# Optimization experiments

Hardware: AMD Instinct MI355X
Metric: run time of the kernel (lower is better)

## Reference

```python
import jax, jax.numpy as jnp
import numpy as np

H = W = 64      # input_resolution
WS = 8          # window_size
NH = 8          # num_heads
C = 256         # dim
HD = C // NH    # head_dim
SCALE = HD ** -0.5
N = WS * WS     # tokens per window
EPS = 1e-5


def _layernorm(x, g, b):
    m = jnp.mean(x, axis=-1, keepdims=True)
    v = jnp.var(x, axis=-1, keepdims=True)
    return (x - m) * jax.lax.rsqrt(v + EPS) * g + b


def _rel_pos_index():
    # Swin relative position index for a WSxWS window -> (N, N) int array
    coords = np.stack(np.meshgrid(np.arange(WS), np.arange(WS), indexing='ij'))  # (2,WS,WS)
    cf = coords.reshape(2, -1)                      # (2, N)
    rel = cf[:, :, None] - cf[:, None, :]           # (2, N, N)
    rel = rel.transpose(1, 2, 0).astype(np.int64)   # (N, N, 2)
    rel[:, :, 0] += WS - 1
    rel[:, :, 1] += WS - 1
    rel[:, :, 0] *= 2 * WS - 1
    return jnp.asarray(rel.sum(-1))                 # (N, N)


def _window_partition(x, B):
    # x: (B, H, W, C) -> (B*nW, N, C)
    x = x.reshape(B, H // WS, WS, W // WS, WS, C)
    x = x.transpose(0, 1, 3, 2, 4, 5)
    return x.reshape(-1, N, C)


def setup_inputs() -> dict:
    key = jax.random.key(0)
    ks = jax.random.split(key, 8)
    B = 16
    std = 0.02
    return {
        'x1': jax.random.normal(ks[0], (B, H * W, C), jnp.float32),
        'x2': jax.random.normal(ks[1], (B, H * W, C), jnp.float32),
        'norm1_g': jnp.ones((C,), jnp.float32),
        'norm1_b': jnp.zeros((C,), jnp.float32),
        'q_w': jax.random.normal(ks[2], (C, C), jnp.float32) * std,
        'q_b': jnp.zeros((C,), jnp.float32),
        'kv_w': jax.random.normal(ks[3], (C, 2 * C), jnp.float32) * std,
        'kv_b': jnp.zeros((2 * C,), jnp.float32),
        'proj_w': jax.random.normal(ks[4], (C, C), jnp.float32) * std,
        'proj_b': jnp.zeros((C,), jnp.float32),
        'rel_table': jax.random.normal(ks[5], ((2 * WS - 1) ** 2, NH), jnp.float32) * std,
        'norm3_g': jnp.ones((C,), jnp.float32),
        'norm3_b': jnp.zeros((C,), jnp.float32),
        'fc1_w': jax.random.normal(ks[6], (C, 4 * C), jnp.float32) * std,
        'fc1_b': jnp.zeros((4 * C,), jnp.float32),
        'fc2_w': jax.random.normal(ks[7], (4 * C, C), jnp.float32) * std,
        'fc2_b': jnp.zeros((C,), jnp.float32),
    }


def reference(x1, x2, norm1_g, norm1_b, q_w, q_b, kv_w, kv_b, proj_w, proj_b,
              rel_table, norm3_g, norm3_b, fc1_w, fc1_b, fc2_w, fc2_b):
    B = x1.shape[0]
    shortcut = x1
    # norm1 applied to both streams (as in source)
    x1n = _layernorm(x1, norm1_g, norm1_b).reshape(B, H, W, C)
    x2n = _layernorm(x2, norm1_g, norm1_b).reshape(B, H, W, C)
    x1w = _window_partition(x1n, B)  # (B_, N, C)
    x2w = _window_partition(x2n, B)  # (B_, N, C)
    B_ = x1w.shape[0]

    q = (x1w @ q_w + q_b).reshape(B_, N, NH, HD).transpose(0, 2, 1, 3)      # (B_,h,N,d)
    kv = (x2w @ kv_w + kv_b).reshape(B_, N, 2, NH, HD)
    k = kv[:, :, 0].transpose(0, 2, 1, 3)                                    # (B_,h,N,d)
    v = kv[:, :, 1].transpose(0, 2, 1, 3)                                    # (B_,h,N,d)

    attn = jnp.einsum('bhnd,bhmd->bhnm', q * SCALE, k)                       # (B_,h,N,N)
    bias = rel_table[_rel_pos_index().reshape(-1)].reshape(N, N, NH)
    attn = jax.nn.softmax(attn + bias.transpose(2, 0, 1)[None], axis=-1)

    out = jnp.einsum('bhnm,bhmd->bhnd', attn, v)
    out = out.transpose(0, 2, 1, 3).reshape(B_, N, C) @ proj_w + proj_b      # (B_,N,C)

    # window reverse -> (B, H*W, C)
    xr = out.reshape(B, H // WS, W // WS, WS, WS, C)
    xr = xr.transpose(0, 1, 3, 2, 4, 5).reshape(B, H * W, C)

    x = shortcut + xr
    h = _layernorm(x, norm3_g, norm3_b)
    h = jax.nn.gelu(h @ fc1_w + fc1_b, approximate=False) @ fc2_w + fc2_b
    return x + h
```

## Files before the change

kernel.cpp:

```cpp
#include <hip/hip_runtime.h>

typedef __bf16 bf16x8 __attribute__((ext_vector_type(8)));
typedef float f32x4 __attribute__((ext_vector_type(4)));
using u16 = unsigned short;

#define SCALE 0.17677669529663689f
#define XROW 528

__device__ __forceinline__ u16 f2bf(float f) {
    union { __bf16 h; u16 u; } x; x.h = (__bf16)f; return x.u;
}
__device__ __forceinline__ unsigned pk2(float a, float b) {
    union { struct { __bf16 lo, hi; } s; unsigned u; } x;
    x.s.lo = (__bf16)a; x.s.hi = (__bf16)b; return x.u;
}
__device__ __forceinline__ float bf2f(u16 h) {
    union { unsigned u; float f; } x; x.u = ((unsigned)h) << 16; return x.f;
}
__device__ __forceinline__ float gelu_s(float x) {
    float u = 2.3022150048054216f * x * (1.f + 0.044715f * x * x);
    float e = exp2f(-u);
    return x / (1.f + e);
}

__global__ __launch_bounds__(256) void prep_k(
    const float* __restrict__ q_w, const float* __restrict__ kv_w,
    const float* __restrict__ p_w, const float* __restrict__ f1w,
    const float* __restrict__ f2w, const float* __restrict__ rel,
    u16* __restrict__ qp, u16* __restrict__ kvp, u16* __restrict__ pp,
    u16* __restrict__ f1p, u16* __restrict__ f2p, float* __restrict__ biasF)
{
    int t = blockIdx.x * 256 + threadIdx.x;
    if (t < 65536) {
        int u = t;
        int e = u & 7, l = (u >> 3) & 63, ks = (u >> 9) & 7, ng = u >> 12;
        int k = ks * 32 + (l >> 4) * 8 + e;
        int n = ng * 16 + (l & 15);
        qp[u] = f2bf(q_w[k * 256 + n]);
    } else if (t < 196608) {
        int u = t - 65536;
        int e = u & 7, l = (u >> 3) & 63, ks = (u >> 9) & 7, ng = u >> 12;
        int k = ks * 32 + (l >> 4) * 8 + e;
        int n = ng * 16 + (l & 15);
        kvp[u] = f2bf(kv_w[k * 512 + n]);
    } else if (t < 262144) {
        int u = t - 196608;
        int e = u & 7, l = (u >> 3) & 63, ks = (u >> 9) & 7, ng = u >> 12;
        int k = ks * 32 + (l >> 4) * 8 + e;
        int n = ng * 16 + (l & 15);
        pp[u] = f2bf(p_w[k * 256 + n]);
    } else if (t < 524288) {
        int u = t - 262144;
        int e = u & 7, l = (u >> 3) & 63, ks = (u >> 9) & 7, ng = u >> 12;
        int k = ks * 32 + (l >> 4) * 8 + e;
        int n = ng * 16 + (l & 15);
        f1p[u] = f2bf(f1w[k * 1024 + n]);
    } else if (t < 786432) {
        int u = t - 524288;
        int e = u & 7, l = (u >> 3) & 63, ks = (u >> 9) & 31, ng = u >> 14;
        int k = ks * 32 + (l >> 4) * 8 + e;
        int n = ng * 16 + (l & 15);
        f2p[u] = f2bf(f2w[k * 256 + n]);
    } else if (t < 819200) {
        int u = t - 786432;
        int r = u & 3, l = (u >> 2) & 63, fr = (u >> 8) & 15, h = u >> 12;
        int fi = fr >> 2, fj = fr & 3;
        int m = fi * 16 + (l & 15);
        int n = fj * 16 + 4 * (l >> 4) + r;
        int idx = ((m >> 3) - (n >> 3) + 7) * 15 + ((m & 7) - (n & 7) + 7);
        biasF[u] = rel[idx * 8 + h];
    }
}

#define LN_ROW16(SRCP, GG, BB, OUT0, OUT1)                                    \
    {                                                                         \
        float4 v0 = *(const float4*)(SRCP);                                   \
        float4 v1 = *(const float4*)(SRCP + 4);                               \
        float4 v2 = *(const float4*)(SRCP + 8);                               \
        float4 v3 = *(const float4*)(SRCP + 12);                              \
        float s = (v0.x + v0.y + v0.z + v0.w) + (v1.x + v1.y + v1.z + v1.w)   \
                + (v2.x + v2.y + v2.z + v2.w) + (v3.x + v3.y + v3.z + v3.w);  \
        float q = v0.x*v0.x + v0.y*v0.y + v0.z*v0.z + v0.w*v0.w               \
                + v1.x*v1.x + v1.y*v1.y + v1.z*v1.z + v1.w*v1.w               \
                + v2.x*v2.x + v2.y*v2.y + v2.z*v2.z + v2.w*v2.w               \
                + v3.x*v3.x + v3.y*v3.y + v3.z*v3.z + v3.w*v3.w;              \
        _Pragma("unroll")                                                     \
        for (int m_ = 1; m_ <= 8; m_ <<= 1) {                                 \
            s += __shfl_xor(s, m_, 64);                                       \
            q += __shfl_xor(q, m_, 64);                                       \
        }                                                                     \
        float mean = s * (1.0f / 256.0f);                                     \
        float rstd = rsqrtf(q * (1.0f / 256.0f) - mean * mean + 1e-5f);       \
        uint4 o0_, o1_;                                                       \
        o0_.x = pk2((v0.x-mean)*rstd*GG[0].x+BB[0].x, (v0.y-mean)*rstd*GG[0].y+BB[0].y); \
        o0_.y = pk2((v0.z-mean)*rstd*GG[0].z+BB[0].z, (v0.w-mean)*rstd*GG[0].w+BB[0].w); \
        o0_.z = pk2((v1.x-mean)*rstd*GG[1].x+BB[1].x, (v1.y-mean)*rstd*GG[1].y+BB[1].y); \
        o0_.w = pk2((v1.z-mean)*rstd*GG[1].z+BB[1].z, (v1.w-mean)*rstd*GG[1].w+BB[1].w); \
        o1_.x = pk2((v2.x-mean)*rstd*GG[2].x+BB[2].x, (v2.y-mean)*rstd*GG[2].y+BB[2].y); \
        o1_.y = pk2((v2.z-mean)*rstd*GG[2].z+BB[2].z, (v2.w-mean)*rstd*GG[2].w+BB[2].w); \
        o1_.z = pk2((v3.x-mean)*rstd*GG[3].x+BB[3].x, (v3.y-mean)*rstd*GG[3].y+BB[3].y); \
        o1_.w = pk2((v3.z-mean)*rstd*GG[3].z+BB[3].z, (v3.w-mean)*rstd*GG[3].w+BB[3].w); \
        OUT0 = o0_; OUT1 = o1_;                                               \
    }

__global__ __launch_bounds__(512, 3) void attn_mega(
    const float* __restrict__ x1, const float* __restrict__ x2,
    const float* __restrict__ gw, const float* __restrict__ bw,
    const bf16x8* __restrict__ qp, const bf16x8* __restrict__ kvp,
    const float* __restrict__ q_b, const float* __restrict__ kv_b,
    const float* __restrict__ biasF, const bf16x8* __restrict__ pp,
    const float* __restrict__ p_b, u16* __restrict__ xbw)
{
    __shared__ __align__(16) char SMEM[74752];
    u16* Xl0  = (u16*)SMEM;
    u16* Xl1  = (u16*)(SMEM + 33792);
    u16* VtA  = (u16*)SMEM;
    u16* Olds = (u16*)(SMEM + 40960);
    const int t = threadIdx.x, lane = t & 63, w = t >> 6;
    const int g = lane >> 4, c = lane & 15;
    const int win = blockIdx.x;
    const int b_ = win >> 6, wh = (win >> 3) & 7, ww = win & 7;

    {
        const int ln_sub = lane >> 4, ln_c = lane & 15;
        float4 GG[4], BB[4];
        #pragma unroll
        for (int j = 0; j < 4; j++) {
            GG[j] = *(const float4*)(gw + ln_c * 16 + j * 4);
            BB[j] = *(const float4*)(bw + ln_c * 16 + j * 4);
        }
        #pragma unroll
        for (int it = 0; it < 4; it++) {
            int idx = w * 16 + it * 4 + ln_sub;
            int st = idx >> 6, n = idx & 63;
            const float* src = st ? x2 : x1;
            size_t srow = (size_t)b_ * 4096 + (wh * 8 + (n >> 3)) * 64 + ww * 8 + (n & 7);
            const float* p = src + srow * 256 + ln_c * 16;
            uint4 o0, o1;
            LN_ROW16(p, GG, BB, o0, o1)
            u16* dst = st ? Xl1 : Xl0;
            char* base = (char*)dst + n * XROW + ln_c * 32;
            *(uint4*)(base) = o0;
            *(uint4*)(base + 16) = o1;
        }
    }
    __syncthreads();

    const int srcA = c + 16 * ((2 * g) & 3);
    const int srcB = srcA + 16;
    const bool nhi = (g >= 2);

#define GEMM256(acc, WPTR, NGBASE, XSRC)                                      \
    { _Pragma("unroll")                                                       \
      for (int i = 0; i < 4; i++) { acc[i][0] = (f32x4){0,0,0,0};             \
                                    acc[i][1] = (f32x4){0,0,0,0}; }           \
      _Pragma("unroll")                                                       \
      for (int ks = 0; ks < 8; ks++) {                                        \
          bf16x8 wf[2], af[4];                                                \
          _Pragma("unroll")                                                   \
          for (int n = 0; n < 2; n++)                                         \
              wf[n] = WPTR[(size_t)(((NGBASE) + n) * 8 + ks) * 64 + lane];    \
          _Pragma("unroll")                                                   \
          for (int i = 0; i < 4; i++)                                         \
              af[i] = *(const bf16x8*)((char*)XSRC + (i * 16 + c) * XROW      \
                                       + g * 16 + ks * 64);                   \
          __builtin_amdgcn_s_setprio(1);                                      \
          _Pragma("unroll")                                                   \
          for (int i = 0; i < 4; i++)                                         \
              _Pragma("unroll")                                               \
              for (int n = 0; n < 2; n++)                                     \
                  acc[i][n] = __builtin_amdgcn_mfma_f32_16x16x32_bf16(        \
                      wf[n], af[i], acc[i][n], 0, 0, 0);                      \
          __builtin_amdgcn_s_setprio(0);                                      \
      } }

#define ADDBIAS(acc, BPTR, CBASE)                                             \
    { _Pragma("unroll")                                                       \
      for (int i = 0; i < 4; i++)                                             \
          _Pragma("unroll")                                                   \
          for (int n = 0; n < 2; n++) {                                       \
              float4 b4 = *(const float4*)((BPTR) + (CBASE) + n * 16 + 4 * g);\
              acc[i][n][0] += b4.x; acc[i][n][1] += b4.y;                     \
              acc[i][n][2] += b4.z; acc[i][n][3] += b4.w;                     \
          } }

#define REPACK(acc, frag)                                                     \
    { unsigned w0_[4][2], w1_[4][2];                                          \
      _Pragma("unroll")                                                       \
      for (int i = 0; i < 4; i++)                                             \
          _Pragma("unroll")                                                   \
          for (int n = 0; n < 2; n++) {                                       \
              w0_[i][n] = pk2(acc[i][n][0], acc[i][n][1]);                    \
              w1_[i][n] = pk2(acc[i][n][2], acc[i][n][3]);                    \
          }                                                                   \
      _Pragma("unroll")                                                       \
      for (int i = 0; i < 4; i++) {                                           \
          unsigned x0a = __shfl(w0_[i][0], srcA), x0b = __shfl(w0_[i][1], srcA);\
          unsigned y0a = __shfl(w1_[i][0], srcA), y0b = __shfl(w1_[i][1], srcA);\
          unsigned x1a = __shfl(w0_[i][0], srcB), x1b = __shfl(w0_[i][1], srcB);\
          unsigned y1a = __shfl(w1_[i][0], srcB), y1b = __shfl(w1_[i][1], srcB);\
          union { uint4 u; bf16x8 v; } cv;                                    \
          cv.u.x = nhi ? x0b : x0a;                                           \
          cv.u.y = nhi ? y0b : y0a;                                           \
          cv.u.z = nhi ? x1b : x1a;                                           \
          cv.u.w = nhi ? y1b : y1a;                                           \
          frag[i] = cv.v;                                                     \
      } }

    bf16x8 qf[4], kf[4];
    f32x4 av[4][2];
    {
        f32x4 acc[4][2];
        GEMM256(acc, kvp, 2 * w, Xl1)
        ADDBIAS(acc, kv_b, w * 32)
        REPACK(acc, kf)
        GEMM256(acc, qp, 2 * w, Xl0)
        ADDBIAS(acc, q_b, w * 32)
        REPACK(acc, qf)
        GEMM256(av, kvp, 16 + 2 * w, Xl1)
        ADDBIAS(av, kv_b, 256 + w * 32)
    }
    __syncthreads();

    u16* vt = VtA + w * 32 * 80;
    #pragma unroll
    for (int i = 0; i < 4; i++)
        #pragma unroll
        for (int n = 0; n < 2; n++)
            #pragma unroll
            for (int r = 0; r < 4; r++)
                vt[(n * 16 + 4 * g + r) * 80 + i * 16 + c] = f2bf(av[i][n][r]);

    f32x4 s[4][4];
    #pragma unroll
    for (int i = 0; i < 4; i++)
        #pragma unroll
        for (int j = 0; j < 4; j++) {
            s[i][j] = (f32x4){0.f, 0.f, 0.f, 0.f};
            s[i][j] = __builtin_amdgcn_mfma_f32_16x16x32_bf16(kf[j], qf[i], s[i][j], 0, 0, 0);
        }

    #pragma unroll
    for (int i = 0; i < 4; i++)
        #pragma unroll
        for (int j = 0; j < 4; j++) {
            f32x4 bf4 = *(const f32x4*)(biasF + ((size_t)(w * 16 + i * 4 + j) * 64 + lane) * 4);
            #pragma unroll
            for (int r = 0; r < 4; r++) s[i][j][r] = s[i][j][r] * SCALE + bf4[r];
        }

    #pragma unroll
    for (int i = 0; i < 4; i++) {
        float mx = -1e30f;
        #pragma unroll
        for (int j = 0; j < 4; j++)
            #pragma unroll
            for (int r = 0; r < 4; r++) mx = fmaxf(mx, s[i][j][r]);
        mx = fmaxf(mx, __shfl_xor(mx, 16, 64));
        mx = fmaxf(mx, __shfl_xor(mx, 32, 64));
        float sum = 0.f;
        #pragma unroll
        for (int j = 0; j < 4; j++)
            #pragma unroll
            for (int r = 0; r < 4; r++) {
                float e = __expf(s[i][j][r] - mx);
                s[i][j][r] = e; sum += e;
            }
        sum += __shfl_xor(sum, 16, 64);
        sum += __shfl_xor(sum, 32, 64);
        float inv = 1.f / sum;
        #pragma unroll
        for (int j = 0; j < 4; j++)
            #pragma unroll
            for (int r = 0; r < 4; r++) s[i][j][r] *= inv;
    }

    unsigned pw0[4][4], pw1[4][4];
    #pragma unroll
    for (int i = 0; i < 4; i++)
        #pragma unroll
        for (int j = 0; j < 4; j++) {
            pw0[i][j] = pk2(s[i][j][0], s[i][j][1]);
            pw1[i][j] = pk2(s[i][j][2], s[i][j][3]);
        }
    f32x4 o[4][2];
    #pragma unroll
    for (int i = 0; i < 4; i++) { o[i][0] = (f32x4){0,0,0,0}; o[i][1] = (f32x4){0,0,0,0}; }
    #pragma unroll
    for (int ks = 0; ks < 2; ks++) {
        bf16x8 pa[4], vb[2];
        #pragma unroll
        for (int i = 0; i < 4; i++) {
            unsigned a0 = __shfl(pw0[i][2 * ks], srcA), b0 = __shfl(pw0[i][2 * ks + 1], srcA);
            unsigned a1 = __shfl(pw1[i][2 * ks], srcA), b1 = __shfl(pw1[i][2 * ks + 1], srcA);
            unsigned a2 = __shfl(pw0[i][2 * ks], srcB), b2 = __shfl(pw0[i][2 * ks + 1], srcB);
            unsigned a3 = __shfl(pw1[i][2 * ks], srcB), b3 = __shfl(pw1[i][2 * ks + 1], srcB);
            union { uint4 u; bf16x8 v; } cv;
            cv.u.x = nhi ? b0 : a0;
            cv.u.y = nhi ? b1 : a1;
            cv.u.z = nhi ? b2 : a2;
            cv.u.w = nhi ? b3 : a3;
            pa[i] = cv.v;
        }
        #pragma unroll
        for (int j = 0; j < 2; j++) {
            int d = j * 16 + c;
            vb[j] = *(const bf16x8*)(vt + d * 80 + ks * 32 + 8 * g);
        }
        #pragma unroll
        for (int i = 0; i < 4; i++)
            #pragma unroll
            for (int j = 0; j < 2; j++)
                o[i][j] = __builtin_amdgcn_mfma_f32_16x16x32_bf16(vb[j], pa[i], o[i][j], 0, 0, 0);
    }

    #pragma unroll
    for (int i = 0; i < 4; i++) {
        int row = i * 16 + c;
        #pragma unroll
        for (int j = 0; j < 2; j++) {
            uint2 pk = { pk2(o[i][j][0], o[i][j][1]), pk2(o[i][j][2], o[i][j][3]) };
            *(uint2*)((char*)Olds + row * XROW + w * 64 + j * 32 + g * 8) = pk;
        }
    }
    __syncthreads();

    f32x4 ap[4][2];
    #pragma unroll
    for (int i = 0; i < 4; i++) { ap[i][0] = (f32x4){0,0,0,0}; ap[i][1] = (f32x4){0,0,0,0}; }
    #pragma unroll
    for (int ks = 0; ks < 8; ks++) {
        bf16x8 wf[2], ah[4];
        #pragma unroll
        for (int n = 0; n < 2; n++)
            wf[n] = pp[(size_t)((w * 2 + n) * 8 + ks) * 64 + lane];
        #pragma unroll
        for (int i = 0; i < 4; i++)
            ah[i] = *(const bf16x8*)((char*)Olds + (i * 16 + c) * XROW
                                     + g * 16 + ks * 64);
        __builtin_amdgcn_s_setprio(1);
        #pragma unroll
        for (int i = 0; i < 4; i++)
            #pragma unroll
            for (int n = 0; n < 2; n++)
                ap[i][n] = __builtin_amdgcn_mfma_f32_16x16x32_bf16(
                    wf[n], ah[i], ap[i][n], 0, 0, 0);
        __builtin_amdgcn_s_setprio(0);
    }

    #pragma unroll
    for (int i = 0; i < 4; i++) {
        int n = i * 16 + c;
        size_t nrow = (size_t)b_ * 4096 + (wh * 8 + (n >> 3)) * 64 + ww * 8 + (n & 7);
        #pragma unroll
        for (int j = 0; j < 2; j++) {
            int col = w * 32 + j * 16 + 4 * g;
            float4 b4 = *(const float4*)(p_b + col);
            float4 r4 = *(const float4*)(x1 + nrow * 256 + col);
            uint2 pk = { pk2(ap[i][j][0] + b4.x + r4.x, ap[i][j][1] + b4.y + r4.y),
                         pk2(ap[i][j][2] + b4.z + r4.z, ap[i][j][3] + b4.w + r4.w) };
            *(uint2*)(xbw + nrow * 256 + col) = pk;
        }
    }
#undef GEMM256
#undef ADDBIAS
#undef REPACK
}

__global__ __launch_bounds__(512, 4) void mlp_mega(
    const u16* __restrict__ xb, const float* __restrict__ gw,
    const float* __restrict__ bw, const bf16x8* __restrict__ f1p,
    const bf16x8* __restrict__ f2p, const float* __restrict__ f1b,
    const float* __restrict__ f2b, float* __restrict__ out)
{
    __shared__ __align__(16) u16 Xl[64 * 264];
    __shared__ __align__(16) u16 Hl[64 * 264];
    const int t = threadIdx.x, lane = t & 63, w = t >> 6;
    const int g = lane >> 4, c = lane & 15;
    const int m0 = blockIdx.x * 64;

    {
        const int ln_sub = lane >> 4, ln_c = lane & 15;
        float4 GG[4], BB[4];
        #pragma unroll
        for (int j = 0; j < 4; j++) {
            GG[j] = *(const float4*)(gw + ln_c * 16 + j * 4);
            BB[j] = *(const float4*)(bw + ln_c * 16 + j * 4);
        }
        #pragma unroll
        for (int it = 0; it < 2; it++) {
            int row = w * 8 + it * 4 + ln_sub;
            const u16* p = xb + (size_t)(m0 + row) * 256 + ln_c * 16;
            uint4 rv = *(const uint4*)(p);
            uint4 rw = *(const uint4*)(p + 8);
            float v[16];
            v[0] = bf2f((u16)rv.x);  v[1] = bf2f((u16)(rv.x >> 16));
            v[2] = bf2f((u16)rv.y);  v[3] = bf2f((u16)(rv.y >> 16));
            v[4] = bf2f((u16)rv.z);  v[5] = bf2f((u16)(rv.z >> 16));
            v[6] = bf2f((u16)rv.w);  v[7] = bf2f((u16)(rv.w >> 16));
            v[8] = bf2f((u16)rw.x);  v[9] = bf2f((u16)(rw.x >> 16));
            v[10] = bf2f((u16)rw.y); v[11] = bf2f((u16)(rw.y >> 16));
            v[12] = bf2f((u16)rw.z); v[13] = bf2f((u16)(rw.z >> 16));
            v[14] = bf2f((u16)rw.w); v[15] = bf2f((u16)(rw.w >> 16));
            float s = 0.f, q = 0.f;
            #pragma unroll
            for (int e = 0; e < 16; e++) { s += v[e]; q += v[e] * v[e]; }
            #pragma unroll
            for (int m_ = 1; m_ <= 8; m_ <<= 1) {
                s += __shfl_xor(s, m_, 64);
                q += __shfl_xor(q, m_, 64);
            }
            float mean = s * (1.0f / 256.0f);
            float rstd = rsqrtf(q * (1.0f / 256.0f) - mean * mean + 1e-5f);
            uint4 o0, o1;
            const float* G = (const float*)GG;
            const float* B = (const float*)BB;
            o0.x = pk2((v[0]-mean)*rstd*G[0]+B[0],  (v[1]-mean)*rstd*G[1]+B[1]);
            o0.y = pk2((v[2]-mean)*rstd*G[2]+B[2],  (v[3]-mean)*rstd*G[3]+B[3]);
            o0.z = pk2((v[4]-mean)*rstd*G[4]+B[4],  (v[5]-mean)*rstd*G[5]+B[5]);
            o0.w = pk2((v[6]-mean)*rstd*G[6]+B[6],  (v[7]-mean)*rstd*G[7]+B[7]);
            o1.x = pk2((v[8]-mean)*rstd*G[8]+B[8],  (v[9]-mean)*rstd*G[9]+B[9]);
            o1.y = pk2((v[10]-mean)*rstd*G[10]+B[10],(v[11]-mean)*rstd*G[11]+B[11]);
            o1.z = pk2((v[12]-mean)*rstd*G[12]+B[12],(v[13]-mean)*rstd*G[13]+B[13]);
            o1.w = pk2((v[14]-mean)*rstd*G[14]+B[14],(v[15]-mean)*rstd*G[15]+B[15]);
            char* base = (char*)Xl + row * XROW + ln_c * 32;
            *(uint4*)(base) = o0;
            *(uint4*)(base + 16) = o1;
        }
    }
    __syncthreads();

    f32x4 acc2[4][2];
    #pragma unroll
    for (int i = 0; i < 4; i++) { acc2[i][0] = (f32x4){0,0,0,0}; acc2[i][1] = (f32x4){0,0,0,0}; }

    #pragma unroll
    for (int hc = 0; hc < 4; hc++) {
        f32x4 acc1[4][2];
        #pragma unroll
        for (int i = 0; i < 4; i++) { acc1[i][0] = (f32x4){0,0,0,0}; acc1[i][1] = (f32x4){0,0,0,0}; }

        const bf16x8* f1base = f1p + (size_t)((hc * 16 + w * 2) * 8) * 64 + lane;
        bf16x8 wA[2], wB[2];
        #pragma unroll
        for (int n = 0; n < 2; n++) wA[n] = f1base[(n * 8 + 0) * 64];

#define FC1_STEP(WREG, ks_)                                                   \
        {                                                                     \
            bf16x8 af[4];                                                     \
            _Pragma("unroll")                                                 \
            for (int i = 0; i < 4; i++)                                       \
                af[i] = *(const bf16x8*)((char*)Xl + (i * 16 + c) * XROW      \
                                         + g * 16 + (ks_) * 64);             \
            __builtin_amdgcn_s_setprio(1);                                    \
            _Pragma("unroll")                                                 \
            for (int i = 0; i < 4; i++)                                       \
                _Pragma("unroll")                                             \
                for (int n = 0; n < 2; n++)                                   \
                    acc1[i][n] = __builtin_amdgcn_mfma_f32_16x16x32_bf16(     \
                        WREG[n], af[i], acc1[i][n], 0, 0, 0);                 \
            __builtin_amdgcn_s_setprio(0);                                    \
        }

        #pragma unroll
        for (int ks = 0; ks < 8; ks += 2) {
            #pragma unroll
            for (int n = 0; n < 2; n++) wB[n] = f1base[(n * 8 + ks + 1) * 64];
            FC1_STEP(wA, ks)
            if (ks + 2 < 8) {
                #pragma unroll
                for (int n = 0; n < 2; n++) wA[n] = f1base[(n * 8 + ks + 2) * 64];
            }
            FC1_STEP(wB, ks + 1)
        }
#undef FC1_STEP

        #pragma unroll
        for (int i = 0; i < 4; i++) {
            int row = i * 16 + c;
            #pragma unroll
            for (int n = 0; n < 2; n++) {
                float4 b4 = *(const float4*)(f1b + hc * 256 + w * 32 + n * 16 + 4 * g);
                float h0 = gelu_s(acc1[i][n][0] + b4.x);
                float h1 = gelu_s(acc1[i][n][1] + b4.y);
                float h2 = gelu_s(acc1[i][n][2] + b4.z);
                float h3 = gelu_s(acc1[i][n][3] + b4.w);
                uint2 pk = { pk2(h0, h1), pk2(h2, h3) };
                *(uint2*)((char*)Hl + row * XROW + w * 64 + n * 32 + g * 8) = pk;
            }
        }
        __syncthreads();

        const bf16x8* f2base = f2p + (size_t)((w * 2) * 32 + hc * 8) * 64 + lane;
        #pragma unroll
        for (int n = 0; n < 2; n++) wA[n] = f2base[(n * 32 + 0) * 64];

#define FC2_STEP(WREG, ks_)                                                   \
        {                                                                     \
            bf16x8 ah[4];                                                     \
            _Pragma("unroll")                                                 \
            for (int i = 0; i < 4; i++)                                       \
                ah[i] = *(const bf16x8*)((char*)Hl + (i * 16 + c) * XROW      \
                                         + g * 16 + (ks_) * 64);             \
            __builtin_amdgcn_s_setprio(1);                                    \
            _Pragma("unroll")                                                 \
            for (int i = 0; i < 4; i++)                                       \
                _Pragma("unroll")                                             \
                for (int n = 0; n < 2; n++)                                   \
                    acc2[i][n] = __builtin_amdgcn_mfma_f32_16x16x32_bf16(     \
                        WREG[n], ah[i], acc2[i][n], 0, 0, 0);                 \
            __builtin_amdgcn_s_setprio(0);                                    \
        }

        #pragma unroll
        for (int ks = 0; ks < 8; ks += 2) {
            #pragma unroll
            for (int n = 0; n < 2; n++) wB[n] = f2base[(n * 32 + ks + 1) * 64];
            FC2_STEP(wA, ks)
            if (ks + 2 < 8) {
                #pragma unroll
                for (int n = 0; n < 2; n++) wA[n] = f2base[(n * 32 + ks + 2) * 64];
            }
            FC2_STEP(wB, ks + 1)
        }
#undef FC2_STEP
        __syncthreads();
    }

    #pragma unroll
    for (int i = 0; i < 4; i++) {
        int row = m0 + i * 16 + c;
        #pragma unroll
        for (int n = 0; n < 2; n++) {
            int col = w * 32 + n * 16 + 4 * g;
            float4 b4 = *(const float4*)(f2b + col);
            uint2 rr = *(const uint2*)(xb + (size_t)row * 256 + col);
            float4 ov = { acc2[i][n][0] + b4.x + bf2f((u16)rr.x),
                          acc2[i][n][1] + b4.y + bf2f((u16)(rr.x >> 16)),
                          acc2[i][n][2] + b4.z + bf2f((u16)rr.y),
                          acc2[i][n][3] + b4.w + bf2f((u16)(rr.y >> 16)) };
            *(float4*)(out + (size_t)row * 256 + col) = ov;
        }
    }
}

extern "C" void kernel_launch(void* const* d_in, const int* in_sizes, int n_in,
                              void* d_out, int out_size, void* d_ws, size_t ws_size,
                              hipStream_t stream)
{
    const float* x1  = (const float*)d_in[0];
    const float* x2  = (const float*)d_in[1];
    const float* n1g = (const float*)d_in[2];
    const float* n1b = (const float*)d_in[3];
    const float* q_w = (const float*)d_in[4];
    const float* q_b = (const float*)d_in[5];
    const float* kv_w= (const float*)d_in[6];
    const float* kv_b= (const float*)d_in[7];
    const float* p_w = (const float*)d_in[8];
    const float* p_b = (const float*)d_in[9];
    const float* rel = (const float*)d_in[10];
    const float* n3g = (const float*)d_in[11];
    const float* n3b = (const float*)d_in[12];
    const float* f1w = (const float*)d_in[13];
    const float* f1b = (const float*)d_in[14];
    const float* f2w = (const float*)d_in[15];
    const float* f2b = (const float*)d_in[16];

    char* ws = (char*)d_ws;
    u16*   qp    = (u16*)(ws + 0);
    u16*   kvp   = (u16*)(ws + 131072);
    u16*   pp    = (u16*)(ws + 393216);
    u16*   f1p   = (u16*)(ws + 524288);
    u16*   f2p   = (u16*)(ws + 1048576);
    float* biasF = (float*)(ws + 1572864);
    u16*   xbw   = (u16*)(ws + 2097152);

    float* out = (float*)d_out;

    prep_k<<<3200, 256, 0, stream>>>(q_w, kv_w, p_w, f1w, f2w, rel,
                                     qp, kvp, pp, f1p, f2p, biasF);
    attn_mega<<<1024, 512, 0, stream>>>(x1, x2, n1g, n1b, (const bf16x8*)qp,
                                        (const bf16x8*)kvp, q_b, kv_b, biasF,
                                        (const bf16x8*)pp, p_b, xbw);
    mlp_mega<<<1024, 512, 0, stream>>>(xbw, n3g, n3b, (const bf16x8*)f1p,
                                       (const bf16x8*)f2p, f1b, f2b, out);
}
```

Baseline: 222.7 us.

## Fuse attention and MLP kernels into one per-window megakernel

```diff
diff --git a/kernel.cpp b/kernel.cpp
--- a/kernel.cpp
+++ b/kernel.cpp
@@ -103,19 +103,25 @@
         OUT0 = o0_; OUT1 = o1_;                                               \
     }
 
-__global__ __launch_bounds__(512, 3) void attn_mega(
+__global__ __launch_bounds__(512, 4) void block_mega(
     const float* __restrict__ x1, const float* __restrict__ x2,
-    const float* __restrict__ gw, const float* __restrict__ bw,
+    const float* __restrict__ n1g, const float* __restrict__ n1b,
     const bf16x8* __restrict__ qp, const bf16x8* __restrict__ kvp,
     const float* __restrict__ q_b, const float* __restrict__ kv_b,
     const float* __restrict__ biasF, const bf16x8* __restrict__ pp,
-    const float* __restrict__ p_b, u16* __restrict__ xbw)
+    const float* __restrict__ p_b,
+    const float* __restrict__ n3g, const float* __restrict__ n3b,
+    const bf16x8* __restrict__ f1p, const bf16x8* __restrict__ f2p,
+    const float* __restrict__ f1b, const float* __restrict__ f2b,
+    float* __restrict__ out)
 {
     __shared__ __align__(16) char SMEM[74752];
     u16* Xl0  = (u16*)SMEM;
     u16* Xl1  = (u16*)(SMEM + 33792);
     u16* VtA  = (u16*)SMEM;
     u16* Olds = (u16*)(SMEM + 40960);
+    u16* Xl4  = (u16*)SMEM;
+    u16* Hl4  = (u16*)(SMEM + 40960);
     const int t = threadIdx.x, lane = t & 63, w = t >> 6;
     const int g = lane >> 4, c = lane & 15;
     const int win = blockIdx.x;
@@ -126,8 +132,8 @@
         float4 GG[4], BB[4];
         #pragma unroll
         for (int j = 0; j < 4; j++) {
-            GG[j] = *(const float4*)(gw + ln_c * 16 + j * 4);
-            BB[j] = *(const float4*)(bw + ln_c * 16 + j * 4);
+            GG[j] = *(const float4*)(n1g + ln_c * 16 + j * 4);
+            BB[j] = *(const float4*)(n1b + ln_c * 16 + j * 4);
         }
         #pragma unroll
         for (int it = 0; it < 4; it++) {
@@ -348,6 +354,7 @@
         __builtin_amdgcn_s_setprio(0);
     }
 
+    uint2 xs[4][2];
     #pragma unroll
     for (int i = 0; i < 4; i++) {
         int n = i * 16 + c;
@@ -359,40 +366,28 @@
             float4 r4 = *(const float4*)(x1 + nrow * 256 + col);
             uint2 pk = { pk2(ap[i][j][0] + b4.x + r4.x, ap[i][j][1] + b4.y + r4.y),
                          pk2(ap[i][j][2] + b4.z + r4.z, ap[i][j][3] + b4.w + r4.w) };
-            *(uint2*)(xbw + nrow * 256 + col) = pk;
-        }
-    }
-#undef GEMM256
-#undef ADDBIAS
-#undef REPACK
-}
-
-__global__ __launch_bounds__(512, 4) void mlp_mega(
-    const u16* __restrict__ xb, const float* __restrict__ gw,
-    const float* __restrict__ bw, const bf16x8* __restrict__ f1p,
-    const bf16x8* __restrict__ f2p, const float* __restrict__ f1b,
-    const float* __restrict__ f2b, float* __restrict__ out)
-{
-    __shared__ __align__(16) u16 Xl[64 * 264];
-    __shared__ __align__(16) u16 Hl[64 * 264];
-    const int t = threadIdx.x, lane = t & 63, w = t >> 6;
-    const int g = lane >> 4, c = lane & 15;
-    const int m0 = blockIdx.x * 64;
+            xs[i][j] = pk;
+            *(uint2*)((char*)Xl4 + (i * 16 + c) * XROW + w * 64 + j * 32 + g * 8) = pk;
+        }
+    }
+    __syncthreads();
 
     {
         const int ln_sub = lane >> 4, ln_c = lane & 15;
-        float4 GG[4], BB[4];
+        float4 G3[4], B3[4];
         #pragma unroll
         for (int j = 0; j < 4; j++) {
-            GG[j] = *(const float4*)(gw + ln_c * 16 + j * 4);
-            BB[j] = *(const float4*)(bw + ln_c * 16 + j * 4);
-        }
+            G3[j] = *(const float4*)(n3g + ln_c * 16 + j * 4);
+            B3[j] = *(const float4*)(n3b + ln_c * 16 + j * 4);
+        }
+        const float* G = (const float*)G3;
+        const float* B = (const float*)B3;
         #pragma unroll
         for (int it = 0; it < 2; it++) {
             int row = w * 8 + it * 4 + ln_sub;
-            const u16* p = xb + (size_t)(m0 + row) * 256 + ln_c * 16;
-            uint4 rv = *(const uint4*)(p);
-            uint4 rw = *(const uint4*)(p + 8);
+            char* base = (char*)Xl4 + row * XROW + ln_c * 32;
+            uint4 rv = *(const uint4*)(base);
+            uint4 rw = *(const uint4*)(base + 16);
             float v[16];
             v[0] = bf2f((u16)rv.x);  v[1] = bf2f((u16)(rv.x >> 16));
             v[2] = bf2f((u16)rv.y);  v[3] = bf2f((u16)(rv.y >> 16));
@@ -402,19 +397,17 @@
             v[10] = bf2f((u16)rw.y); v[11] = bf2f((u16)(rw.y >> 16));
             v[12] = bf2f((u16)rw.z); v[13] = bf2f((u16)(rw.z >> 16));
             v[14] = bf2f((u16)rw.w); v[15] = bf2f((u16)(rw.w >> 16));
-            float s = 0.f, q = 0.f;
-            #pragma unroll
-            for (int e = 0; e < 16; e++) { s += v[e]; q += v[e] * v[e]; }
+            float sm = 0.f, qm = 0.f;
+            #pragma unroll
+            for (int e = 0; e < 16; e++) { sm += v[e]; qm += v[e] * v[e]; }
             #pragma unroll
             for (int m_ = 1; m_ <= 8; m_ <<= 1) {
-                s += __shfl_xor(s, m_, 64);
-                q += __shfl_xor(q, m_, 64);
+                sm += __shfl_xor(sm, m_, 64);
+                qm += __shfl_xor(qm, m_, 64);
             }
-            float mean = s * (1.0f / 256.0f);
-            float rstd = rsqrtf(q * (1.0f / 256.0f) - mean * mean + 1e-5f);
+            float mean = sm * (1.0f / 256.0f);
+            float rstd = rsqrtf(qm * (1.0f / 256.0f) - mean * mean + 1e-5f);
             uint4 o0, o1;
-            const float* G = (const float*)GG;
-            const float* B = (const float*)BB;
             o0.x = pk2((v[0]-mean)*rstd*G[0]+B[0],  (v[1]-mean)*rstd*G[1]+B[1]);
             o0.y = pk2((v[2]-mean)*rstd*G[2]+B[2],  (v[3]-mean)*rstd*G[3]+B[3]);
             o0.z = pk2((v[4]-mean)*rstd*G[4]+B[4],  (v[5]-mean)*rstd*G[5]+B[5]);
@@ -423,7 +416,6 @@
             o1.y = pk2((v[10]-mean)*rstd*G[10]+B[10],(v[11]-mean)*rstd*G[11]+B[11]);
             o1.z = pk2((v[12]-mean)*rstd*G[12]+B[12],(v[13]-mean)*rstd*G[13]+B[13]);
             o1.w = pk2((v[14]-mean)*rstd*G[14]+B[14],(v[15]-mean)*rstd*G[15]+B[15]);
-            char* base = (char*)Xl + row * XROW + ln_c * 32;
             *(uint4*)(base) = o0;
             *(uint4*)(base + 16) = o1;
         }
@@ -450,7 +442,7 @@
             bf16x8 af[4];                                                     \
             _Pragma("unroll")                                                 \
             for (int i = 0; i < 4; i++)                                       \
-                af[i] = *(const bf16x8*)((char*)Xl + (i * 16 + c) * XROW      \
+                af[i] = *(const bf16x8*)((char*)Xl4 + (i * 16 + c) * XROW     \
                                          + g * 16 + (ks_) * 64);             \
             __builtin_amdgcn_s_setprio(1);                                    \
             _Pragma("unroll")                                                 \
@@ -486,7 +478,7 @@
                 float h2 = gelu_s(acc1[i][n][2] + b4.z);
                 float h3 = gelu_s(acc1[i][n][3] + b4.w);
                 uint2 pk = { pk2(h0, h1), pk2(h2, h3) };
-                *(uint2*)((char*)Hl + row * XROW + w * 64 + n * 32 + g * 8) = pk;
+                *(uint2*)((char*)Hl4 + row * XROW + w * 64 + n * 32 + g * 8) = pk;
             }
         }
         __syncthreads();
@@ -500,7 +492,7 @@
             bf16x8 ah[4];                                                     \
             _Pragma("unroll")                                                 \
             for (int i = 0; i < 4; i++)                                       \
-                ah[i] = *(const bf16x8*)((char*)Hl + (i * 16 + c) * XROW      \
+                ah[i] = *(const bf16x8*)((char*)Hl4 + (i * 16 + c) * XROW     \
                                          + g * 16 + (ks_) * 64);             \
             __builtin_amdgcn_s_setprio(1);                                    \
             _Pragma("unroll")                                                 \
@@ -529,19 +521,23 @@
 
     #pragma unroll
     for (int i = 0; i < 4; i++) {
-        int row = m0 + i * 16 + c;
-        #pragma unroll
-        for (int n = 0; n < 2; n++) {
-            int col = w * 32 + n * 16 + 4 * g;
+        int n = i * 16 + c;
+        size_t nrow = (size_t)b_ * 4096 + (wh * 8 + (n >> 3)) * 64 + ww * 8 + (n & 7);
+        #pragma unroll
+        for (int j = 0; j < 2; j++) {
+            int col = w * 32 + j * 16 + 4 * g;
             float4 b4 = *(const float4*)(f2b + col);
-            uint2 rr = *(const uint2*)(xb + (size_t)row * 256 + col);
-            float4 ov = { acc2[i][n][0] + b4.x + bf2f((u16)rr.x),
-                          acc2[i][n][1] + b4.y + bf2f((u16)(rr.x >> 16)),
-                          acc2[i][n][2] + b4.z + bf2f((u16)rr.y),
-                          acc2[i][n][3] + b4.w + bf2f((u16)(rr.y >> 16)) };
-            *(float4*)(out + (size_t)row * 256 + col) = ov;
-        }
-    }
+            uint2 rr = xs[i][j];
+            float4 ov = { acc2[i][j][0] + b4.x + bf2f((u16)rr.x),
+                          acc2[i][j][1] + b4.y + bf2f((u16)(rr.x >> 16)),
+                          acc2[i][j][2] + b4.z + bf2f((u16)rr.y),
+                          acc2[i][j][3] + b4.w + bf2f((u16)(rr.y >> 16)) };
+            *(float4*)(out + nrow * 256 + col) = ov;
+        }
+    }
+#undef GEMM256
+#undef ADDBIAS
+#undef REPACK
 }
 
 extern "C" void kernel_launch(void* const* d_in, const int* in_sizes, int n_in,
@@ -573,15 +569,14 @@
     u16*   f1p   = (u16*)(ws + 524288);
     u16*   f2p   = (u16*)(ws + 1048576);
     float* biasF = (float*)(ws + 1572864);
-    u16*   xbw   = (u16*)(ws + 2097152);
 
     float* out = (float*)d_out;
 
     prep_k<<<3200, 256, 0, stream>>>(q_w, kv_w, p_w, f1w, f2w, rel,
                                      qp, kvp, pp, f1p, f2p, biasF);
-    attn_mega<<<1024, 512, 0, stream>>>(x1, x2, n1g, n1b, (const bf16x8*)qp,
-                                        (const bf16x8*)kvp, q_b, kv_b, biasF,
-                                        (const bf16x8*)pp, p_b, xbw);
-    mlp_mega<<<1024, 512, 0, stream>>>(xbw, n3g, n3b, (const bf16x8*)f1p,
-                                       (const bf16x8*)f2p, f1b, f2b, out);
-}
+    block_mega<<<1024, 512, 0, stream>>>(x1, x2, n1g, n1b, (const bf16x8*)qp,
+                                         (const bf16x8*)kvp, q_b, kv_b, biasF,
+                                         (const bf16x8*)pp, p_b, n3g, n3b,
+                                         (const bf16x8*)f1p, (const bf16x8*)f2p,
+                                         f1b, f2b, out);
+}
```

Result: faster. 202.1 us (-9.2%).
